# Kernel optimization log

Measured on AMD Instinct MI355X. Metric: run time of the kernel, lower is better.

## Reference

```python
import jax, jax.numpy as jnp
import numpy as np


def setup_inputs() -> dict:
    key = jax.random.key(0)
    ks = jax.random.split(key, 7)
    B, S, E, N, H = 2, 2048, 1024, 8, 4096
    scale = 0.02
    return {
        "x": jax.random.normal(ks[0], (B, S, E), dtype=jnp.float32),
        "Wr": jax.random.normal(ks[1], (E, N), dtype=jnp.float32) * scale,
        "br": jnp.zeros((N,), dtype=jnp.float32),
        "W1": jax.random.normal(ks[2], (N, E, H), dtype=jnp.float32) * scale,
        "b1": jnp.zeros((N, H), dtype=jnp.float32),
        "W2": jax.random.normal(ks[3], (N, H, E), dtype=jnp.float32) * scale,
        "b2": jnp.zeros((N, E), dtype=jnp.float32),
        "top_k": 2,
    }


def reference(x, Wr, br, W1, b1, W2, b2, top_k):
    # Router: logits [B,S,N], keep top-k, softmax over the kept entries.
    logits = jnp.einsum("bse,en->bsn", x, Wr) + br
    _, idx = jax.lax.top_k(logits, top_k)                      # [B,S,k]
    mask = jax.nn.one_hot(idx, logits.shape[-1], dtype=jnp.bool_).any(-2)  # [B,S,N]
    masked = jnp.where(mask, logits, -jnp.inf)
    weights = jax.nn.softmax(masked, axis=-1)                   # [B,S,N]

    # Dense all-experts FFN (faithful to original): every expert on every token.
    # hid: [B,S,N,H]
    hid = jax.nn.gelu(jnp.einsum("bse,neh->bsnh", x, W1) + b1, approximate=False)
    expert_out = jnp.einsum("bsnh,nhe->bsne", hid, W2) + b2    # [B,S,N,E]
    # dropout is identity in eval mode

    # Weighted combine over experts.
    return jnp.einsum("bsne,bsn->bse", expert_out, weights)
```

## Files before the change

### kernel.cpp

```cpp
#include <hip/hip_runtime.h>
#include <hip/hip_bf16.h>
#include <cmath>
#include <cstdint>


typedef unsigned short u16;
typedef __attribute__((ext_vector_type(8))) short bf16x8;
typedef __attribute__((ext_vector_type(4))) float f32x4;
typedef __attribute__((ext_vector_type(8))) unsigned short us8;
typedef __attribute__((ext_vector_type(4))) unsigned short us4;

#define TOKENS  4096
#define EDIM    1024
#define NEXP    8
#define HDIM    4096
#define MAXROWS 8192
#define ROWPAD  128
#define MAXTILES 72
#define RBLK    1024

#define MFMA16(va, vb, vc) __builtin_amdgcn_mfma_f32_16x16x32_bf16(va, vb, vc, 0, 0, 0)

__device__ __forceinline__ u16 f2bf(float f) {
  __hip_bfloat16 h = __float2bfloat16(f);
  return *reinterpret_cast<u16*>(&h);
}
__device__ __forceinline__ int clampk(int k) {
  return k < 1 ? 1 : (k > 8 ? 8 : k);
}
__device__ __forceinline__ void async16(void* lds, const void* g) {
  __builtin_amdgcn_global_load_lds((const __attribute__((address_space(1))) void*)g,
                                   (__attribute__((address_space(3))) void*)lds,
                                   16, 0, 0);
}
__device__ __forceinline__ float gelu_f(float v) {
  const float z = fabsf(v) * 0.70710678118654752f;
  const float t = __builtin_amdgcn_rcpf(fmaf(0.3275911f, z, 1.0f));
  const float p = t * fmaf(t, fmaf(t, fmaf(t, fmaf(t, 1.061405429f, -1.453152027f),
                                           1.421413741f), -0.284496736f), 0.254829592f);
  float er = 1.0f - p * __expf(-z * z);
  er = copysignf(er, v);
  return 0.5f * v * (1.0f + er);
}

__global__ void router_k(const float* __restrict__ x, const float* __restrict__ Wr,
                         const float* __restrict__ br, const int* __restrict__ topk_p,
                         int* __restrict__ sel_e, float* __restrict__ sel_w,
                         int* __restrict__ sel_lpos, int* __restrict__ hist_blk) {
  __shared__ int wsel[4][8];
  const int blk = blockIdx.x;
  const int tid = threadIdx.x;
  const int wv = tid >> 6, ln = tid & 63;
  const int t = blk * 4 + wv;
  const int k = clampk(topk_p[0]);
  float acc[NEXP];
#pragma unroll
  for (int n = 0; n < NEXP; ++n) acc[n] = 0.f;
  const float* xr = x + (size_t)t * EDIM;
  for (int ei = ln; ei < EDIM; ei += 64) {
    float xv = xr[ei];
    float4 w0 = *(const float4*)(Wr + ei * NEXP);
    float4 w1 = *(const float4*)(Wr + ei * NEXP + 4);
    acc[0] += xv * w0.x; acc[1] += xv * w0.y; acc[2] += xv * w0.z; acc[3] += xv * w0.w;
    acc[4] += xv * w1.x; acc[5] += xv * w1.y; acc[6] += xv * w1.z; acc[7] += xv * w1.w;
  }
#pragma unroll
  for (int s = 32; s > 0; s >>= 1) {
#pragma unroll
    for (int n = 0; n < NEXP; ++n) acc[n] += __shfl_down(acc[n], s);
  }
  if (ln == 0) {
    float logit[NEXP];
#pragma unroll
    for (int n = 0; n < NEXP; ++n) logit[n] = acc[n] + br[n];
    bool used[NEXP];
#pragma unroll
    for (int n = 0; n < NEXP; ++n) used[n] = false;
    int se[NEXP]; float sw[NEXP];
    for (int j = 0; j < k; ++j) {
      int bi = 0; float bv = -INFINITY;
      for (int n = 0; n < NEXP; ++n)
        if (!used[n] && logit[n] > bv) { bv = logit[n]; bi = n; }
      used[bi] = true; se[j] = bi; sw[j] = bv;
    }
    float mx = sw[0], sum = 0.f;
    for (int j = 0; j < k; ++j) { sw[j] = expf(sw[j] - mx); sum += sw[j]; }
    float inv = 1.f / sum;
    for (int j = 0; j < k; ++j) {
      sel_e[t * 8 + j] = se[j];
      sel_w[t * 8 + j] = sw[j] * inv;
      wsel[wv][j] = se[j];
    }
  }
  __syncthreads();
  if (tid == 0) {
    int h[NEXP];
#pragma unroll
    for (int e = 0; e < NEXP; ++e) h[e] = 0;
    for (int w = 0; w < 4; ++w)
      for (int j = 0; j < k; ++j) {
        int e = wsel[w][j];
        sel_lpos[(blk * 4 + w) * 8 + j] = h[e]++;
      }
#pragma unroll
    for (int e = 0; e < NEXP; ++e) hist_blk[blk * NEXP + e] = h[e];
  }
}

__global__ void scan_k(const int* __restrict__ hist_blk, int* __restrict__ counts,
                       int* __restrict__ offsets, int* __restrict__ blk_base,
                       int* __restrict__ tmap) {
  __shared__ int sc[NEXP][257];
  __shared__ int offs[NEXP];
  const int tid = threadIdx.x;
  int h[4][NEXP], part[NEXP];
#pragma unroll
  for (int e = 0; e < NEXP; ++e) part[e] = 0;
#pragma unroll
  for (int r = 0; r < 4; ++r) {
    const int row = tid * 4 + r;
#pragma unroll
    for (int e = 0; e < NEXP; ++e) { h[r][e] = hist_blk[row * NEXP + e]; part[e] += h[r][e]; }
  }
#pragma unroll
  for (int e = 0; e < NEXP; ++e) sc[e][tid] = part[e];
  __syncthreads();
  for (int d = 1; d < 256; d <<= 1) {
    int v[NEXP];
#pragma unroll
    for (int e = 0; e < NEXP; ++e) v[e] = (tid >= d) ? sc[e][tid - d] : 0;
    __syncthreads();
#pragma unroll
    for (int e = 0; e < NEXP; ++e) sc[e][tid] += v[e];
    __syncthreads();
  }
  if (tid == 0) {
    int s = 0;
    for (int e = 0; e < NEXP; ++e) {
      int tot = sc[e][255];
      offsets[e] = s; offs[e] = s; counts[e] = tot; s += tot;
    }
    int nt = 0;
    for (int e = 0; e < NEXP; ++e) {
      int nb = (counts[e] + 127) >> 7;
      for (int b = 0; b < nb && nt < MAXTILES; ++b) tmap[nt++] = (e << 16) | b;
    }
    for (; nt < MAXTILES; ++nt) tmap[nt] = -1;
  }
  __syncthreads();
#pragma unroll
  for (int e = 0; e < NEXP; ++e) {
    int run = offs[e] + sc[e][tid] - part[e];
#pragma unroll
    for (int r = 0; r < 4; ++r) {
      blk_base[(tid * 4 + r) * NEXP + e] = run;
      run += h[r][e];
    }
  }
}

__global__ void finalize_k(const int* __restrict__ sel_e, const int* __restrict__ sel_lpos,
                           const int* __restrict__ blk_base, const int* __restrict__ topk_p,
                           int* __restrict__ sel_pos, int* __restrict__ row_token) {
  const int k = clampk(topk_p[0]);
  const int i = blockIdx.x * 256 + threadIdx.x;
  if (i >= TOKENS * k) return;
  const int t = i / k, j = i - t * k;
  const int e = sel_e[t * 8 + j];
  const int pos = blk_base[(t >> 2) * NEXP + e] + sel_lpos[t * 8 + j];
  sel_pos[t * 8 + j] = pos;
  row_token[pos] = t;
}

__global__ void gather_cast_k(const float* __restrict__ x, const int* __restrict__ row_token,
                              const int* __restrict__ counts, u16* __restrict__ xg) {
  __shared__ int tot_s;
  if (threadIdx.x == 0) {
    int t = 0;
#pragma unroll
    for (int e = 0; e < NEXP; ++e) t += counts[e];
    tot_s = t;
  }
  __syncthreads();
  const int row = blockIdx.x;
  u16* dst = xg + (size_t)row * EDIM;
  const int i = threadIdx.x;
  if (row >= tot_s) {
    us4 z = {0, 0, 0, 0};
    *(us4*)(dst + i * 4) = z;
    return;
  }
  const float* src = x + (size_t)row_token[row] * EDIM;
  float4 v = *(const float4*)(src + i * 4);
  us4 o; o[0] = f2bf(v.x); o[1] = f2bf(v.y); o[2] = f2bf(v.z); o[3] = f2bf(v.w);
  *(us4*)(dst + i * 4) = o;
}

__global__ void transpose_k(const float* __restrict__ W1, const float* __restrict__ W2,
                            u16* __restrict__ W1t, u16* __restrict__ W2t,
                            int full, int h0c) {
  __shared__ __align__(16) u16 T[64][68];
  const int z = blockIdx.z;
  int mat, e, h0;
  if (full) { mat = z < 32 ? 0 : 1; int zz = mat ? z - 32 : z; e = zz >> 2; h0 = (zz & 3) * 1024; }
  else      { mat = z < 8 ? 0 : 1;  e = mat ? z - 8 : z;      h0 = h0c; }
  const size_t oes = full ? (size_t)HDIM * EDIM : (size_t)1024 * 1024;
  const float* in; size_t istride;
  if (mat == 0) { in = W1 + (size_t)e * EDIM * HDIM + h0;            istride = HDIM; }
  else          { in = W2 + (size_t)e * HDIM * EDIM + (size_t)h0 * EDIM; istride = EDIM; }
  const int r0 = blockIdx.y * 64, c0 = blockIdx.x * 64;
  const int tid = threadIdx.x;
#pragma unroll
  for (int it = 0; it < 4; ++it) {
    int cell = it * 256 + tid;
    int rl = cell >> 4, c4 = (cell & 15) * 4;
    float4 v = *(const float4*)(in + (size_t)(r0 + rl) * istride + c0 + c4);
    us4 o; o[0] = f2bf(v.x); o[1] = f2bf(v.y); o[2] = f2bf(v.z); o[3] = f2bf(v.w);
    *(us4*)&T[rl][c4] = o;
  }
  __syncthreads();
#pragma unroll
  for (int it = 0; it < 2; ++it) {
    int cell = it * 256 + tid;
    int cl = cell >> 3, r8 = (cell & 7) * 8;
    us8 o;
#pragma unroll
    for (int j = 0; j < 8; ++j) o[j] = T[r8 + j][cl];
    u16* out;
    if (mat == 0) {
      int orow = (full ? h0 : 0) + c0 + cl;
      out = W1t + (size_t)e * oes + (size_t)orow * 1024 + r0 + r8;
    } else {
      int ost = full ? HDIM : 1024;
      out = W2t + (size_t)e * oes + (size_t)(c0 + cl) * ost + (full ? h0 : 0) + r0 + r8;
    }
    *(us8*)out = o;
  }
}

template <int MODE>
__global__ __launch_bounds__(256, 3) void gemm_k(
    const u16* __restrict__ A, int astride, int kblocks,
    const u16* __restrict__ Bt, size_t b_estride, int bstride,
    const float* __restrict__ bias, int bias_dim, int bias_col0, int bias_on,
    const int* __restrict__ counts, const int* __restrict__ offsets,
    const int* __restrict__ tmap, int NB,
    u16* __restrict__ hid, int hid_stride, float* __restrict__ Y, int accum) {
  __shared__ __align__(16) u16 As[128 * 64];
  __shared__ __align__(16) u16 Bs[128 * 64];
  const int bid = blockIdx.x;
  const int tile = bid / NB;
  const int tv = tmap[tile];
  if (tv < 0) return;
  const int n0 = (bid - tile * NB) << 7;
  const int e = tv >> 16;
  const int m0 = (tv & 0xffff) << 7;
  const int cnt = counts[e], off_e = offsets[e];

  const int tid = threadIdx.x;
  const int wv = tid >> 6, ln = tid & 63;
  const int wm = wv >> 1, wn = wv & 1;

  const int trow = tid >> 3;
  const int swz  = (tid & 7) ^ (trow & 7);
  const u16* gA = A + (size_t)(off_e + m0 + trow) * astride + swz * 8;
  const u16* gB = Bt + (size_t)e * b_estride + (size_t)(n0 + trow) * bstride + swz * 8;
  const size_t a32 = (size_t)astride * 32;
  const size_t b32 = (size_t)bstride * 32;
  u16* const lA = As + wv * 512;
  u16* const lB = Bs + wv * 512;

  const int r15 = ln & 15, quad = ln >> 4, rs = r15 & 7;
  const int arow = (wm * 64 + r15) * 64;
  const int brow = (wn * 64 + r15) * 64;
  const int s0 = (quad ^ rs) * 8;
  const int s1 = ((quad + 4) ^ rs) * 8;

  f32x4 acc[4][4];
#pragma unroll
  for (int i = 0; i < 4; ++i)
#pragma unroll
    for (int j = 0; j < 4; ++j) acc[i][j] = (f32x4){0.f, 0.f, 0.f, 0.f};

  for (int kb = 0; kb < kblocks; ++kb) {
    const int k0 = kb * 64;
    __syncthreads();
    const u16* ga = gA + k0;
    const u16* gb = gB + k0;
#pragma unroll
    for (int h = 0; h < 4; ++h) async16(lA + h * 2048, ga + (size_t)h * a32);
#pragma unroll
    for (int h = 0; h < 4; ++h) async16(lB + h * 2048, gb + (size_t)h * b32);
    __syncthreads();

    bf16x8 a0[4], a1[4], b0[4], b1[4];
#pragma unroll
    for (int mi = 0; mi < 4; ++mi) {
      a0[mi] = *(const bf16x8*)(As + arow + mi * 1024 + s0);
      a1[mi] = *(const bf16x8*)(As + arow + mi * 1024 + s1);
    }
#pragma unroll
    for (int ni = 0; ni < 4; ++ni) {
      b0[ni] = *(const bf16x8*)(Bs + brow + ni * 1024 + s0);
      b1[ni] = *(const bf16x8*)(Bs + brow + ni * 1024 + s1);
    }
#pragma unroll
    for (int mi = 0; mi < 4; ++mi)
#pragma unroll
      for (int ni = 0; ni < 4; ++ni) {
        acc[mi][ni] = MFMA16(a0[mi], b0[ni], acc[mi][ni]);
        acc[mi][ni] = MFMA16(a1[mi], b1[ni], acc[mi][ni]);
      }
  }

  const int col0 = n0 + wn * 64 + r15;
  float bv[4];
#pragma unroll
  for (int ni = 0; ni < 4; ++ni) {
    const float b = bias[(size_t)e * bias_dim + bias_col0 + col0 + ni * 16];
    bv[ni] = (MODE == 0) ? b : (bias_on ? b : 0.f);
  }
#pragma unroll
  for (int mi = 0; mi < 4; ++mi) {
    const int mb = m0 + wm * 64 + mi * 16 + quad * 4;
#pragma unroll
    for (int ni = 0; ni < 4; ++ni) {
      const int nc = col0 + ni * 16;
#pragma unroll
      for (int r = 0; r < 4; ++r) {
        const int m = mb + r;
        if (m < cnt) {
          const float v = acc[mi][ni][r] + bv[ni];
          if (MODE == 0) {
            hid[(size_t)(off_e + m) * hid_stride + nc] = f2bf(gelu_f(v));
          } else {
            size_t yi = (size_t)(off_e + m) * EDIM + nc;
            Y[yi] = accum ? (Y[yi] + v) : v;
          }
        }
      }
    }
  }
}

__global__ void combine_k(const float* __restrict__ Y, const int* __restrict__ sel_pos,
                          const float* __restrict__ sel_w, const int* __restrict__ topk_p,
                          float* __restrict__ out) {
  const int t = blockIdx.x;
  const int tid = threadIdx.x;
  const int k = clampk(topk_p[0]);
  float a0 = 0.f, a1 = 0.f, a2 = 0.f, a3 = 0.f;
  for (int j = 0; j < k; ++j) {
    const float w = sel_w[t * 8 + j];
    const size_t row = (size_t)sel_pos[t * 8 + j];
    const float4 v = *(const float4*)(Y + row * EDIM + tid * 4);
    a0 += w * v.x; a1 += w * v.y; a2 += w * v.z; a3 += w * v.w;
  }
  float4 o; o.x = a0; o.y = a1; o.z = a2; o.w = a3;
  *(float4*)(out + (size_t)t * EDIM + tid * 4) = o;
}

extern "C" void kernel_launch(void* const* d_in, const int* in_sizes, int n_in,
                              void* d_out, int out_size, void* d_ws, size_t ws_size,
                              hipStream_t stream) {
  const float* x   = (const float*)d_in[0];
  const float* Wr  = (const float*)d_in[1];
  const float* br  = (const float*)d_in[2];
  const float* W1  = (const float*)d_in[3];
  const float* b1  = (const float*)d_in[4];
  const float* W2  = (const float*)d_in[5];
  const float* b2  = (const float*)d_in[6];
  const int* topk  = (const int*)d_in[7];
  float* out = (float*)d_out;

  char* ws = (char*)d_ws;
  size_t o = 0;
  auto alloc = [&](size_t bytes) -> char* {
    char* p = ws + o; o += (bytes + 255) & ~(size_t)255; return p;
  };
  int*   counts    = (int*)alloc(NEXP * 4);
  int*   offsets   = (int*)alloc(NEXP * 4);
  int*   tmap      = (int*)alloc(MAXTILES * 4);
  int*   sel_e     = (int*)alloc((size_t)TOKENS * 8 * 4);
  int*   sel_pos   = (int*)alloc((size_t)TOKENS * 8 * 4);
  int*   sel_lpos  = (int*)alloc((size_t)TOKENS * 8 * 4);
  float* sel_w     = (float*)alloc((size_t)TOKENS * 8 * 4);
  int*   row_token = (int*)alloc((size_t)TOKENS * 8 * 4);
  int*   hist_blk  = (int*)alloc((size_t)RBLK * NEXP * 4);
  int*   blk_base  = (int*)alloc((size_t)RBLK * NEXP * 4);
  u16*   xg        = (u16*)alloc((size_t)(MAXROWS + ROWPAD) * EDIM * 2);
  float* Y         = (float*)alloc((size_t)MAXROWS * EDIM * 4);

  const size_t full_need  = ((size_t)NEXP * HDIM * EDIM * 2) * 2
                          + (size_t)(MAXROWS + ROWPAD) * HDIM * 2 + 4096;
  const bool full = (ws_size - o) >= full_need;
  u16 *W1t, *W2t, *hid;
  if (full) {
    W1t = (u16*)alloc((size_t)NEXP * HDIM * EDIM * 2);
    W2t = (u16*)alloc((size_t)NEXP * HDIM * EDIM * 2);
    hid = (u16*)alloc((size_t)(MAXROWS + ROWPAD) * HDIM * 2);
  } else {
    W1t = (u16*)alloc((size_t)NEXP * 1024 * 1024 * 2);
    W2t = (u16*)alloc((size_t)NEXP * 1024 * 1024 * 2);
    hid = (u16*)alloc((size_t)(MAXROWS + ROWPAD) * 1024 * 2);
  }

  router_k<<<dim3(RBLK), dim3(256), 0, stream>>>(x, Wr, br, topk,
                                                 sel_e, sel_w, sel_lpos, hist_blk);
  scan_k<<<dim3(1), dim3(256), 0, stream>>>(hist_blk, counts, offsets, blk_base, tmap);
  finalize_k<<<dim3(TOKENS * 8 / 256), dim3(256), 0, stream>>>(sel_e, sel_lpos, blk_base,
                                                               topk, sel_pos, row_token);
  gather_cast_k<<<dim3(MAXROWS + ROWPAD), dim3(256), 0, stream>>>(x, row_token, counts, xg);

  if (full) {
    transpose_k<<<dim3(16, 16, 64), dim3(256), 0, stream>>>(W1, W2, W1t, W2t, 1, 0);
    gemm_k<0><<<dim3(MAXTILES * 32), dim3(256), 0, stream>>>(
        xg, EDIM, 16, W1t, (size_t)HDIM * EDIM, 1024,
        b1, HDIM, 0, 1, counts, offsets, tmap, 32, hid, HDIM, nullptr, 0);
    gemm_k<1><<<dim3(MAXTILES * 8), dim3(256), 0, stream>>>(
        hid, HDIM, 64, W2t, (size_t)HDIM * EDIM, HDIM,
        b2, EDIM, 0, 1, counts, offsets, tmap, 8, nullptr, 0, Y, 0);
  } else {
    for (int c = 0; c < 4; ++c) {
      const int h0 = c * 1024;
      transpose_k<<<dim3(16, 16, 16), dim3(256), 0, stream>>>(W1, W2, W1t, W2t, 0, h0);
      gemm_k<0><<<dim3(MAXTILES * 8), dim3(256), 0, stream>>>(
          xg, EDIM, 16, W1t, (size_t)1024 * 1024, 1024,
          b1, HDIM, h0, 1, counts, offsets, tmap, 8, hid, 1024, nullptr, 0);
      gemm_k<1><<<dim3(MAXTILES * 8), dim3(256), 0, stream>>>(
          hid, 1024, 16, W2t, (size_t)1024 * 1024, 1024,
          b2, EDIM, 0, (c == 0) ? 1 : 0, counts, offsets, tmap, 8, nullptr, 0, Y,
          (c == 0) ? 0 : 1);
    }
  }
  combine_k<<<dim3(TOKENS), dim3(256), 0, stream>>>(Y, sel_pos, sel_w, topk, out);
}
```

Measured before the change: 567.8 us.

## Split-K the second expert GEMM with atomic accumulation into zeroed output

The down-projection GEMM in the full-workspace path now splits its K dimension (hidden size) into two halves across blockIdx.y and accumulates partial results into Y with atomicAdd. Only the first split adds the bias. Y is zeroed inside the gather kernel so the atomics start from zero. This doubles the number of blocks for a GEMM that only had about 8 column tiles per row tile, which should fill the GPU better, at the cost of atomic traffic and extra Y zeroing writes. The transpose LDS tile is also repadded to 66 columns, with its stores split into 2-element writes to change the bank-conflict pattern.

Measured after the change: 596.3 us. 5.0% more time.

```diff
diff --git a/kernel.cpp b/kernel.cpp
--- a/kernel.cpp
+++ b/kernel.cpp
@@ -9,6 +9,7 @@
 typedef __attribute__((ext_vector_type(4))) float f32x4;
 typedef __attribute__((ext_vector_type(8))) unsigned short us8;
 typedef __attribute__((ext_vector_type(4))) unsigned short us4;
+typedef __attribute__((ext_vector_type(2))) unsigned short us2;
 
 #define TOKENS  4096
 #define EDIM    1024
@@ -173,7 +174,8 @@
 }
 
 __global__ void gather_cast_k(const float* __restrict__ x, const int* __restrict__ row_token,
-                              const int* __restrict__ counts, u16* __restrict__ xg) {
+                              const int* __restrict__ counts, u16* __restrict__ xg,
+                              float* __restrict__ Y) {
   __shared__ int tot_s;
   if (threadIdx.x == 0) {
     int t = 0;
@@ -181,10 +183,14 @@
     for (int e = 0; e < NEXP; ++e) t += counts[e];
     tot_s = t;
   }
+  const int row = blockIdx.x;
+  const int i = threadIdx.x;
+  if (row < MAXROWS) {
+    float4 z = {0.f, 0.f, 0.f, 0.f};
+    *(float4*)(Y + (size_t)row * EDIM + i * 4) = z;
+  }
   __syncthreads();
-  const int row = blockIdx.x;
   u16* dst = xg + (size_t)row * EDIM;
-  const int i = threadIdx.x;
   if (row >= tot_s) {
     us4 z = {0, 0, 0, 0};
     *(us4*)(dst + i * 4) = z;
@@ -199,7 +205,7 @@
 __global__ void transpose_k(const float* __restrict__ W1, const float* __restrict__ W2,
                             u16* __restrict__ W1t, u16* __restrict__ W2t,
                             int full, int h0c) {
-  __shared__ __align__(16) u16 T[64][68];
+  __shared__ u16 T[64][66];
   const int z = blockIdx.z;
   int mat, e, h0;
   if (full) { mat = z < 32 ? 0 : 1; int zz = mat ? z - 32 : z; e = zz >> 2; h0 = (zz & 3) * 1024; }
@@ -215,8 +221,10 @@
     int cell = it * 256 + tid;
     int rl = cell >> 4, c4 = (cell & 15) * 4;
     float4 v = *(const float4*)(in + (size_t)(r0 + rl) * istride + c0 + c4);
-    us4 o; o[0] = f2bf(v.x); o[1] = f2bf(v.y); o[2] = f2bf(v.z); o[3] = f2bf(v.w);
-    *(us4*)&T[rl][c4] = o;
+    us2 lo; lo[0] = f2bf(v.x); lo[1] = f2bf(v.y);
+    us2 hi; hi[0] = f2bf(v.z); hi[1] = f2bf(v.w);
+    *(us2*)&T[rl][c4]     = lo;
+    *(us2*)&T[rl][c4 + 2] = hi;
   }
   __syncthreads();
 #pragma unroll
@@ -245,10 +253,12 @@
     const float* __restrict__ bias, int bias_dim, int bias_col0, int bias_on,
     const int* __restrict__ counts, const int* __restrict__ offsets,
     const int* __restrict__ tmap, int NB,
-    u16* __restrict__ hid, int hid_stride, float* __restrict__ Y, int accum) {
+    u16* __restrict__ hid, int hid_stride, float* __restrict__ Y,
+    int accum, int atomic_acc) {
   __shared__ __align__(16) u16 As[128 * 64];
   __shared__ __align__(16) u16 Bs[128 * 64];
   const int bid = blockIdx.x;
+  const int by  = blockIdx.y;
   const int tile = bid / NB;
   const int tv = tmap[tile];
   if (tv < 0) return;
@@ -263,8 +273,9 @@
 
   const int trow = tid >> 3;
   const int swz  = (tid & 7) ^ (trow & 7);
-  const u16* gA = A + (size_t)(off_e + m0 + trow) * astride + swz * 8;
-  const u16* gB = Bt + (size_t)e * b_estride + (size_t)(n0 + trow) * bstride + swz * 8;
+  const size_t koff = (size_t)by * kblocks * 64;
+  const u16* gA = A + (size_t)(off_e + m0 + trow) * astride + koff + swz * 8;
+  const u16* gB = Bt + (size_t)e * b_estride + (size_t)(n0 + trow) * bstride + koff + swz * 8;
   const size_t a32 = (size_t)astride * 32;
   const size_t b32 = (size_t)bstride * 32;
   u16* const lA = As + wv * 512;
@@ -318,7 +329,7 @@
 #pragma unroll
   for (int ni = 0; ni < 4; ++ni) {
     const float b = bias[(size_t)e * bias_dim + bias_col0 + col0 + ni * 16];
-    bv[ni] = (MODE == 0) ? b : (bias_on ? b : 0.f);
+    bv[ni] = (MODE == 0) ? b : ((bias_on && by == 0) ? b : 0.f);
   }
 #pragma unroll
   for (int mi = 0; mi < 4; ++mi) {
@@ -335,7 +346,8 @@
             hid[(size_t)(off_e + m) * hid_stride + nc] = f2bf(gelu_f(v));
           } else {
             size_t yi = (size_t)(off_e + m) * EDIM + nc;
-            Y[yi] = accum ? (Y[yi] + v) : v;
+            if (atomic_acc)  atomicAdd(&Y[yi], v);
+            else             Y[yi] = accum ? (Y[yi] + v) : v;
           }
         }
       }
@@ -410,27 +422,28 @@
   scan_k<<<dim3(1), dim3(256), 0, stream>>>(hist_blk, counts, offsets, blk_base, tmap);
   finalize_k<<<dim3(TOKENS * 8 / 256), dim3(256), 0, stream>>>(sel_e, sel_lpos, blk_base,
                                                                topk, sel_pos, row_token);
-  gather_cast_k<<<dim3(MAXROWS + ROWPAD), dim3(256), 0, stream>>>(x, row_token, counts, xg);
+  gather_cast_k<<<dim3(MAXROWS + ROWPAD), dim3(256), 0, stream>>>(x, row_token, counts,
+                                                                  xg, Y);
 
   if (full) {
     transpose_k<<<dim3(16, 16, 64), dim3(256), 0, stream>>>(W1, W2, W1t, W2t, 1, 0);
-    gemm_k<0><<<dim3(MAXTILES * 32), dim3(256), 0, stream>>>(
+    gemm_k<0><<<dim3(MAXTILES * 32, 1), dim3(256), 0, stream>>>(
         xg, EDIM, 16, W1t, (size_t)HDIM * EDIM, 1024,
-        b1, HDIM, 0, 1, counts, offsets, tmap, 32, hid, HDIM, nullptr, 0);
-    gemm_k<1><<<dim3(MAXTILES * 8), dim3(256), 0, stream>>>(
-        hid, HDIM, 64, W2t, (size_t)HDIM * EDIM, HDIM,
-        b2, EDIM, 0, 1, counts, offsets, tmap, 8, nullptr, 0, Y, 0);
+        b1, HDIM, 0, 1, counts, offsets, tmap, 32, hid, HDIM, nullptr, 0, 0);
+    gemm_k<1><<<dim3(MAXTILES * 8, 2), dim3(256), 0, stream>>>(
+        hid, HDIM, 32, W2t, (size_t)HDIM * EDIM, HDIM,
+        b2, EDIM, 0, 1, counts, offsets, tmap, 8, nullptr, 0, Y, 0, 1);
   } else {
     for (int c = 0; c < 4; ++c) {
       const int h0 = c * 1024;
       transpose_k<<<dim3(16, 16, 16), dim3(256), 0, stream>>>(W1, W2, W1t, W2t, 0, h0);
-      gemm_k<0><<<dim3(MAXTILES * 8), dim3(256), 0, stream>>>(
+      gemm_k<0><<<dim3(MAXTILES * 8, 1), dim3(256), 0, stream>>>(
           xg, EDIM, 16, W1t, (size_t)1024 * 1024, 1024,
-          b1, HDIM, h0, 1, counts, offsets, tmap, 8, hid, 1024, nullptr, 0);
-      gemm_k<1><<<dim3(MAXTILES * 8), dim3(256), 0, stream>>>(
+          b1, HDIM, h0, 1, counts, offsets, tmap, 8, hid, 1024, nullptr, 0, 0);
+      gemm_k<1><<<dim3(MAXTILES * 8, 1), dim3(256), 0, stream>>>(
           hid, 1024, 16, W2t, (size_t)1024 * 1024, 1024,
           b2, EDIM, 0, (c == 0) ? 1 : 0, counts, offsets, tmap, 8, nullptr, 0, Y,
-          (c == 0) ? 0 : 1);
+          (c == 0) ? 0 : 1, 0);
     }
   }
   combine_k<<<dim3(TOKENS), dim3(256), 0, stream>>>(Y, sel_pos, sel_w, topk, out);
```
